# Kernel tuning notes

Hardware: AMD Instinct MI355X
Metric: run time of the kernel (lower is better)

The kernel has to match this reference:

```python
import jax, jax.numpy as jnp
import numpy as np


def setup_inputs() -> dict:
    key = jax.random.key(0)
    k1, k2 = jax.random.split(key)
    N, C, H, W = 1, 32, 128, 240
    return {
        "left_feature": jax.random.normal(k1, (N, C, H, W), dtype=jnp.float32),
        "right_feature": jax.random.normal(k2, (N, C, H, W), dtype=jnp.float32),
        "max_disparity": 192,
    }


def reference(left_feature, right_feature, max_disparity):
    # left_feature, right_feature: (N, C, H, W)
    N, C, H, W = left_feature.shape
    D4 = max_disparity // 4
    i_idx = jnp.arange(D4)[:, None]          # (D4, 1) disparity index
    w_idx = jnp.arange(W)[None, :]           # (1, W)  column index
    valid = (w_idx >= i_idx)                 # (D4, W): cols written at disparity i
    m = valid[None, None, :, None, :]        # (1, 1, D4, 1, W)

    # Left half: cost[:, :C, i, :, i:] = left[:, :, :, i:] (unshifted, masked)
    left_vol = jnp.where(m, left_feature[:, :, None, :, :], jnp.zeros((), left_feature.dtype))

    # Right half: cost[:, C:, i, :, i:] = right[:, :, :, :-i] -> right shifted by i
    shift = jnp.clip(w_idx - i_idx, 0, W - 1)              # (D4, W)
    right_sh = right_feature[:, :, :, shift]               # (N, C, H, D4, W)
    right_vol = jnp.where(m, jnp.transpose(right_sh, (0, 1, 3, 2, 4)),
                          jnp.zeros((), right_feature.dtype))

    # (N, 2C, D4, H, W)
    return jnp.concatenate([left_vol, right_vol], axis=1)
```

## Files before the change

kernel.cpp:

```cpp
#include <hip/hip_runtime.h>


constexpr int C  = 32;
constexpr int H  = 128;
constexpr int W  = 240;
constexpr int D4 = 48;
constexpr int W4 = W / 4;
constexpr int TOTAL4 = 2 * C * D4 * H * W4;

typedef float f32x4 __attribute__((ext_vector_type(4)));

__global__ void __launch_bounds__(256) cost_volume_kernel(
    const float* __restrict__ left,
    const float* __restrict__ right,
    float* __restrict__ out) {
    const int stride = gridDim.x * blockDim.x;
    for (int idx = blockIdx.x * blockDim.x + threadIdx.x; idx < TOTAL4;
         idx += stride) {
        int w4 = idx % W4;
        int t  = idx / W4;
        int h  = t % H;
        t /= H;
        int d = t % D4;
        int c = t / D4;

        const int w0 = w4 * 4;
        const bool is_left = (c < C);
        const float* __restrict__ src =
            is_left ? (left + (c * H + h) * W)
                    : (right + ((c - C) * H + h) * W);
        const int shift = is_left ? 0 : d;

        f32x4 vec;
#pragma unroll
        for (int j = 0; j < 4; ++j) {
            const int wj = w0 + j;
            vec[j] = (wj >= d) ? src[wj - shift] : 0.0f;
        }

        __builtin_nontemporal_store(vec, reinterpret_cast<f32x4*>(out) + idx);
    }
}

extern "C" void kernel_launch(void* const* d_in, const int* in_sizes, int n_in,
                              void* d_out, int out_size, void* d_ws,
                              size_t ws_size, hipStream_t stream) {
    const float* left  = (const float*)d_in[0];
    const float* right = (const float*)d_in[1];
    float* out = (float*)d_out;

    const int block = 256;
    const int grid  = 2048;
    cost_volume_kernel<<<grid, block, 0, stream>>>(left, right, out);
}
```

Before: 93.26 us.

## Stage each input row in padded LDS and reuse it across all disparities

The grid-stride loop is replaced with one block per (channel, row) pair. Each block loads its source row into shared memory once, padded to avoid bank conflicts, and four waves write all 48 disparity slices from it. This removes the per-element div/mod index math and the repeated unaligned global reads. The kernel is write-bound, so the gain is expected to be modest, and only 60 of each wave's 64 lanes are active.

```diff
diff --git a/kernel.cpp b/kernel.cpp
--- a/kernel.cpp
+++ b/kernel.cpp
@@ -6,39 +6,49 @@
 constexpr int W  = 240;
 constexpr int D4 = 48;
 constexpr int W4 = W / 4;
-constexpr int TOTAL4 = 2 * C * D4 * H * W4;
 
 typedef float f32x4 __attribute__((ext_vector_type(4)));
+
+__device__ __forceinline__ int pidx(int w) { return w + (w >> 5); }
 
 __global__ void __launch_bounds__(256) cost_volume_kernel(
     const float* __restrict__ left,
     const float* __restrict__ right,
     float* __restrict__ out) {
-    const int stride = gridDim.x * blockDim.x;
-    for (int idx = blockIdx.x * blockDim.x + threadIdx.x; idx < TOTAL4;
-         idx += stride) {
-        int w4 = idx % W4;
-        int t  = idx / W4;
-        int h  = t % H;
-        t /= H;
-        int d = t % D4;
-        int c = t / D4;
+    __shared__ float row[W + (W >> 5)];
 
-        const int w0 = w4 * 4;
-        const bool is_left = (c < C);
-        const float* __restrict__ src =
-            is_left ? (left + (c * H + h) * W)
-                    : (right + ((c - C) * H + h) * W);
+    const int blk = blockIdx.x;
+    const int h   = blk & (H - 1);
+    const int c2  = blk >> 7;
+    const bool is_left = (c2 < C);
+    const float* __restrict__ src =
+        is_left ? (left  + (c2 * H + h) * W)
+                : (right + ((c2 - C) * H + h) * W);
+
+    const int tid = threadIdx.x;
+    if (tid < W) row[pidx(tid)] = src[tid];
+    __syncthreads();
+
+    const int lane = tid & 63;
+    const int wave = tid >> 6;
+    if (lane >= W4) return;
+
+    const int w0 = lane * 4;
+    f32x4* __restrict__ out4 = reinterpret_cast<f32x4*>(out);
+    const int base    = (c2 * D4 * H + h) * W4 + lane;
+    const int dstride = H * W4;
+
+#pragma unroll
+    for (int pass = 0; pass < D4 / 4; ++pass) {
+        const int d     = pass * 4 + wave;
         const int shift = is_left ? 0 : d;
-
-        f32x4 vec;
+        f32x4 v;
 #pragma unroll
         for (int j = 0; j < 4; ++j) {
             const int wj = w0 + j;
-            vec[j] = (wj >= d) ? src[wj - shift] : 0.0f;
+            v[j] = (wj >= d) ? row[pidx(wj - shift)] : 0.0f;
         }
-
-        __builtin_nontemporal_store(vec, reinterpret_cast<f32x4*>(out) + idx);
+        __builtin_nontemporal_store(v, out4 + base + d * dstride);
     }
 }
 
@@ -49,7 +59,7 @@
     const float* right = (const float*)d_in[1];
     float* out = (float*)d_out;
 
+    const int grid  = 2 * C * H;
     const int block = 256;
-    const int grid  = 2048;
     cost_volume_kernel<<<grid, block, 0, stream>>>(left, right, out);
 }
```

Result: faster. 77.43 us (-17.0%).
